# Kernel tuning notes

Measured on AMD Instinct MI355X. Metric: run time of the kernel, lower is better.

The kernel has to match this reference:

```python
import jax, jax.numpy as jnp
import numpy as np

EMBED = 1024
HEAD = 128

def setup_inputs() -> dict:
    key = jax.random.key(0)
    k1, k2, k3, k4 = jax.random.split(key, 4)
    x = jax.random.normal(k1, (4, 4096, EMBED), dtype=jnp.float32)
    # nn.Linear default init ~ U(-1/sqrt(fan_in), 1/sqrt(fan_in)); weights stored as [in, out] for x @ W
    s = 1.0 / np.sqrt(EMBED)
    Wq = jax.random.uniform(k2, (EMBED, HEAD), dtype=jnp.float32, minval=-s, maxval=s)
    Wk = jax.random.uniform(k3, (EMBED, HEAD), dtype=jnp.float32, minval=-s, maxval=s)
    Wv = jax.random.uniform(k4, (EMBED, HEAD), dtype=jnp.float32, minval=-s, maxval=s)
    return {"x": x, "Wq": Wq, "Wk": Wk, "Wv": Wv}

def reference(x, Wq, Wk, Wv):
    # x: [B, S, E]
    B, S, E = x.shape
    q = x @ Wq  # [B, S, H]
    k = x @ Wk
    v = x @ Wv
    scale = jnp.asarray(k.shape[-1], x.dtype) ** -0.5
    scores = jnp.einsum('bqh,bkh->bqk', q, k) * scale  # [B, S, S]
    causal = jnp.tril(jnp.ones((S, S), dtype=bool))
    scores = jnp.where(causal, scores, jnp.asarray(-jnp.inf, x.dtype))
    attn = jax.nn.softmax(scores, axis=-1)
    return jnp.einsum('bqk,bkh->bqh', attn, v)  # [B, S, H]
```

## Files before the change

kernel.cpp:

```cpp
#include <hip/hip_runtime.h>
#include <math.h>

#define BATCH 4
#define SEQ   4096
#define EMB   1024
#define HD    128
#define MROWS (BATCH*SEQ)
#define SCALE  0.08838834764831844f
#define SCALEQ 0.12751742f
#define CHUNK 10
#define NJOBS 119
#define MAXC  7

typedef __attribute__((ext_vector_type(8))) short bf16x8;
typedef __attribute__((ext_vector_type(4))) short short4v;
typedef __attribute__((ext_vector_type(4))) float f32x4;
typedef __attribute__((ext_vector_type(4))) int   i32x4;
typedef __attribute__((ext_vector_type(2))) int   i32x2;

static __device__ __forceinline__ unsigned short f2bf(float f) {
    unsigned int u = __float_as_uint(f);
    u += 0x7fff + ((u >> 16) & 1);
    return (unsigned short)(u >> 16);
}
static __device__ __forceinline__ float bf2f(unsigned short s) {
    return __uint_as_float((unsigned int)s << 16);
}
static __device__ __forceinline__ short4v pack4(float4 a) {
    short4v p;
    p[0] = (short)f2bf(a.x); p[1] = (short)f2bf(a.y);
    p[2] = (short)f2bf(a.z); p[3] = (short)f2bf(a.w);
    return p;
}
static __device__ __forceinline__ int cvtpk(float lo, float hi) {
    int r;
    asm("v_cvt_pk_bf16_f32 %0, %1, %2" : "=v"(r) : "v"(lo), "v"(hi));
    return r;
}
static __device__ __forceinline__ void gload_lds16(const unsigned short* g, unsigned short* l) {
    __builtin_amdgcn_global_load_lds(
        (const __attribute__((address_space(1))) void*)g,
        (__attribute__((address_space(3))) void*)l, 16, 0, 0);
}

__global__ __launch_bounds__(256) void wtrans_kernel(
    const float* __restrict__ Wq, const float* __restrict__ Wk,
    const float* __restrict__ Wv, unsigned short* __restrict__ Wt)
{
    __shared__ __align__(16) unsigned short Xs[16 * 132];
    const int w  = blockIdx.y;
    const float* W = (w == 0) ? Wq : (w == 1) ? Wk : Wv;
    const float sc = (w == 0) ? SCALEQ : 1.0f;
    const int bx = blockIdx.x;
    const int k0 = bx * 16;
    const int t  = threadIdx.x;

#pragma unroll
    for (int i = 0; i < 2; ++i) {
        int gg = i * 256 + t;
        int row = gg >> 5, c4 = gg & 31;
        float4 a = *(const float4*)&W[(size_t)(k0 + row) * HD + c4 * 4];
        short4v p;
        p[0] = (short)f2bf(a.x * sc); p[1] = (short)f2bf(a.y * sc);
        p[2] = (short)f2bf(a.z * sc); p[3] = (short)f2bf(a.w * sc);
        *(short4v*)&Xs[row * 132 + c4 * 4] = p;
    }
    __syncthreads();
    const int n = t >> 1, g = t & 1;
    i32x4 o;
#pragma unroll
    for (int e = 0; e < 4; ++e) {
        unsigned int lo = Xs[(g * 8 + e * 2    ) * 132 + n];
        unsigned int hi = Xs[(g * 8 + e * 2 + 1) * 132 + n];
        o[e] = (int)(lo | (hi << 16));
    }
    const int ntg  = w * 8 + (n >> 4);
    const int kc   = bx >> 1;
    const int quad = (bx * 2 + g) & 3;
    const int lane = quad * 16 + (n & 15);
    *(i32x4*)&Wt[(((size_t)ntg * 32 + kc) * 64 + lane) * 8] = o;
}

__global__ __launch_bounds__(512, 2) void qkv_kernel(
    const float* __restrict__ x, const unsigned short* __restrict__ Wt,
    unsigned short* __restrict__ qb, unsigned short* __restrict__ kb,
    unsigned short* __restrict__ vtb)
{
    __shared__ __align__(1024) unsigned short lds[58368];
    unsigned short* Ws  = lds;
    unsigned short* xsA = lds + 49152;
    unsigned short* xsB = lds + 53760;

    const int t    = threadIdx.x;
    const int lane = t & 63, ng = t >> 6;
    const int quad = lane >> 4, l16 = lane & 15;
    const int m0   = blockIdx.x * 64;

    f32x4 acc[4][3];
#pragma unroll
    for (int i = 0; i < 4; ++i)
#pragma unroll
        for (int j = 0; j < 3; ++j) acc[i][j] = (f32x4){0.f, 0.f, 0.f, 0.f};

    const int xr0 = t >> 4,         xc0 = (t & 15) * 4;
    const int xr1 = (t + 512) >> 4, xc1 = ((t + 512) & 15) * 4;
    const float* xb0 = x + (size_t)(m0 + xr0) * EMB + xc0;
    const float* xb1 = x + (size_t)(m0 + xr1) * EMB + xc1;

    const unsigned short* Wg = Wt + (size_t)lane * 8;
    float4 xra, xrb;

    {
        float4 a = *(const float4*)&xb0[0];
        float4 b = *(const float4*)&xb1[0];
        *(short4v*)&xsA[xr0 * 72 + xc0] = pack4(a);
        *(short4v*)&xsA[xr1 * 72 + xc1] = pack4(b);
#pragma unroll
        for (int jt = 0; jt < 3; ++jt)
#pragma unroll
            for (int kcl = 0; kcl < 2; ++kcl) {
                int ntg = ng * 3 + jt;
                gload_lds16(Wg + ((size_t)ntg * 32 + kcl) * 512,
                            Ws + ((size_t)ntg * 2 + kcl) * 512);
            }
        xra = *(const float4*)&xb0[64];
        xrb = *(const float4*)&xb1[64];
    }
    asm volatile("s_waitcnt vmcnt(2)" ::: "memory");
    asm volatile("s_waitcnt lgkmcnt(0)" ::: "memory");
    __builtin_amdgcn_s_barrier();

    for (int ph = 0; ph < 16; ++ph) {
        const int cb = ph & 1, nb = cb ^ 1;
        unsigned short* xc = cb ? xsB : xsA;
        unsigned short* xn = cb ? xsA : xsB;
        const int kcn = (ph < 15 ? ph + 1 : 15) * 2;

#pragma unroll
        for (int jt = 0; jt < 3; ++jt)
#pragma unroll
            for (int kcl = 0; kcl < 2; ++kcl) {
                int ntg = ng * 3 + jt;
                gload_lds16(Wg + ((size_t)ntg * 32 + kcn + kcl) * 512,
                            Ws + ((size_t)(nb * 48) + ntg * 2 + kcl) * 512);
            }
        *(short4v*)&xn[xr0 * 72 + xc0] = pack4(xra);
        *(short4v*)&xn[xr1 * 72 + xc1] = pack4(xrb);
        {
            const int xcol = (ph + 2 < 16) ? (ph + 2) * 64 : 960;
            xra = *(const float4*)&xb0[xcol];
            xrb = *(const float4*)&xb1[xcol];
        }
        {
            bf16x8 aA[2][4], aB[2][3];
#pragma unroll
            for (int ks = 0; ks < 2; ++ks)
#pragma unroll
                for (int jt = 0; jt < 3; ++jt)
                    aB[ks][jt] = *(const bf16x8*)&Ws[((size_t)(cb * 48) + (ng * 3 + jt) * 2 + ks) * 512 + lane * 8];
#pragma unroll
            for (int ks = 0; ks < 2; ++ks)
#pragma unroll
                for (int mt = 0; mt < 4; ++mt)
                    aA[ks][mt] = *(const bf16x8*)&xc[(mt * 16 + l16) * 72 + ks * 32 + quad * 8];
            __builtin_amdgcn_s_setprio(1);
#pragma unroll
            for (int ks = 0; ks < 2; ++ks)
#pragma unroll
                for (int mt = 0; mt < 4; ++mt)
#pragma unroll
                    for (int jt = 0; jt < 3; ++jt)
                        acc[mt][jt] = __builtin_amdgcn_mfma_f32_16x16x32_bf16(
                            aA[ks][mt], aB[ks][jt], acc[mt][jt], 0, 0, 0);
            __builtin_amdgcn_s_setprio(0);
        }
        asm volatile("s_waitcnt vmcnt(2)" ::: "memory");
        asm volatile("s_waitcnt lgkmcnt(0)" ::: "memory");
        __builtin_amdgcn_s_barrier();
    }

    unsigned short* Cq = lds;
    unsigned short* Ck = lds + 64 * 136;
    unsigned short* Cv = lds + 2 * 64 * 136;
#pragma unroll
    for (int mt = 0; mt < 4; ++mt)
#pragma unroll
        for (int jt = 0; jt < 3; ++jt) {
            int nt = ng * 3 + jt;
            int wm = nt >> 3, nl = nt & 7;
            if (wm < 2) {
                unsigned short* C = (wm == 0) ? Cq : Ck;
#pragma unroll
                for (int rr = 0; rr < 4; ++rr)
                    C[(mt * 16 + quad * 4 + rr) * 136 + nl * 16 + l16] =
                        f2bf(acc[mt][jt][rr]);
            } else {
                i32x2 p;
                p[0] = cvtpk(acc[mt][jt][0], acc[mt][jt][1]);
                p[1] = cvtpk(acc[mt][jt][2], acc[mt][jt][3]);
                *(i32x2*)&Cv[(nl * 16 + l16) * 72 + mt * 16 + quad * 4] = p;
            }
        }
    __syncthreads();
    {
#pragma unroll
        for (int i = 0; i < 2; ++i) {
            int idx = i * 512 + t;
            int row = idx >> 4, seg = idx & 15;
            *(i32x4*)&qb[((size_t)(m0 + row)) * HD + seg * 8] = *(const i32x4*)&Cq[row * 136 + seg * 8];
            *(i32x4*)&kb[((size_t)(m0 + row)) * HD + seg * 8] = *(const i32x4*)&Ck[row * 136 + seg * 8];
        }
    }
    {
        const int b = m0 >> 12, s0 = m0 & 4095;
#pragma unroll
        for (int i = 0; i < 2; ++i) {
            int idx = i * 512 + t;
            int h = idx >> 3, seg = idx & 7;
            *(i32x4*)&vtb[(size_t)b * (HD * SEQ) + (size_t)h * SEQ + s0 + seg * 8] =
                *(const i32x4*)&Cv[h * 72 + seg * 8];
        }
    }
}

#define PADK 136
#define PADV 72
#define PADP 72
#define DEFER_THR 8.0f

__global__ __launch_bounds__(256, 2) void flash_kernel(
    const unsigned short* __restrict__ qb, const unsigned short* __restrict__ kb,
    const unsigned short* __restrict__ vtb, unsigned short* __restrict__ Opart,
    float* __restrict__ mbuf, float* __restrict__ lbuf)
{
    __shared__ __align__(16) unsigned short Ks[64 * PADK];
    __shared__ __align__(16) unsigned short Vt[128 * PADV];
    __shared__ __align__(16) unsigned short Pt[128 * PADP];

    const int bx   = blockIdx.x;
    const int slot = bx & 7, pp = bx >> 3;
    const int b    = slot >> 1;
    const int jj   = pp * 2 + (slot & 1);
    if (jj >= NJOBS) return;

    const int t    = threadIdx.x;
    const int lane = t & 63, w = t >> 6;
    const int quad = lane >> 4, l16 = lane & 15;

    int qi = 0, s = 0;
    for (qi = 0; qi < 32; ++qi) {
        int cnt = (qi + 5) / 5;
        if (jj < s + cnt) break;
        s += cnt;
    }
    const int c     = jj - s;
    const int qrow0 = qi * 128 + w * 32 + l16;
    const int qrow1 = qrow0 + 16;
    const int jmax  = 2 * qi + 2;
    const int jbeg  = c * CHUNK;
    const int jend  = min(jbeg + CHUNK, jmax);
    const int wtop  = qi * 128 + w * 32;

    bf16x8 qf0[4], qf1[4];
    {
        const unsigned short* qp0 = qb + ((size_t)b * SEQ + qrow0) * HD;
        const unsigned short* qp1 = qb + ((size_t)b * SEQ + qrow1) * HD;
#pragma unroll
        for (int ks = 0; ks < 4; ++ks) {
            qf0[ks] = *(const bf16x8*)&qp0[ks * 32 + quad * 8];
            qf1[ks] = *(const bf16x8*)&qp1[ks * 32 + quad * 8];
        }
    }

    f32x4 O0[8], O1[8];
#pragma unroll
    for (int i = 0; i < 8; ++i) {
        O0[i] = (f32x4){0.f, 0.f, 0.f, 0.f};
        O1[i] = (f32x4){0.f, 0.f, 0.f, 0.f};
    }
    float m0r = -1e30f, l0r = 0.f, m1r = -1e30f, l1r = 0.f;

    const unsigned short* kbb  = kb  + (size_t)b * SEQ * HD;
    const unsigned short* vtbb = vtb + (size_t)b * HD * SEQ;

    i32x4 kr[4], vr[4];
#pragma unroll
    for (int i = 0; i < 4; ++i) {
        int gg = i * 256 + t;
        kr[i] = *(const i32x4*)&kbb[(size_t)jbeg * 64 * HD + (size_t)gg * 8];
        vr[i] = *(const i32x4*)&vtbb[(size_t)(gg >> 3) * SEQ + jbeg * 64 + (gg & 7) * 8];
    }

    for (int j0 = jbeg; j0 < jend; ++j0) {
        __syncthreads();
#pragma unroll
        for (int i = 0; i < 4; ++i) {
            int gg = i * 256 + t;
            *(i32x4*)&Ks[(gg >> 4) * PADK + (gg & 15) * 8] = kr[i];
            *(i32x4*)&Vt[(gg >> 3) * PADV + (gg & 7) * 8] = vr[i];
        }
        __syncthreads();

        if (j0 + 1 < jend) {
            const int j1 = j0 + 1;
#pragma unroll
            for (int i = 0; i < 4; ++i) {
                int gg = i * 256 + t;
                kr[i] = *(const i32x4*)&kbb[(size_t)j1 * 64 * HD + (size_t)gg * 8];
                vr[i] = *(const i32x4*)&vtbb[(size_t)(gg >> 3) * SEQ + j1 * 64 + (gg & 7) * 8];
            }
        }

        if (j0 * 64 > wtop + 31) continue;

        f32x4 st0[4], st1[4];
#pragma unroll
        for (int mt = 0; mt < 4; ++mt) {
            st0[mt] = (f32x4){0.f, 0.f, 0.f, 0.f};
            st1[mt] = (f32x4){0.f, 0.f, 0.f, 0.f};
        }
        __builtin_amdgcn_s_setprio(1);
#pragma unroll
        for (int mt = 0; mt < 4; ++mt)
#pragma unroll
            for (int ks = 0; ks < 4; ++ks) {
                bf16x8 kf = *(const bf16x8*)&Ks[(mt * 16 + l16) * PADK + ks * 32 + quad * 8];
                st0[mt] = __builtin_amdgcn_mfma_f32_16x16x32_bf16(kf, qf0[ks], st0[mt], 0, 0, 0);
                st1[mt] = __builtin_amdgcn_mfma_f32_16x16x32_bf16(kf, qf1[ks], st1[mt], 0, 0, 0);
            }
        __builtin_amdgcn_s_setprio(0);

        if (j0 * 64 + 63 > wtop) {
#pragma unroll
            for (int mt = 0; mt < 4; ++mt)
#pragma unroll
                for (int rr = 0; rr < 4; ++rr) {
                    int kv = j0 * 64 + mt * 16 + quad * 4 + rr;
                    if (kv > qrow0) st0[mt][rr] = -1e30f;
                    if (kv > qrow1) st1[mt][rr] = -1e30f;
                }
        }

        {
            float mx = -1e30f;
#pragma unroll
            for (int mt = 0; mt < 4; ++mt)
#pragma unroll
                for (int rr = 0; rr < 4; ++rr) mx = fmaxf(mx, st0[mt][rr]);
            mx = fmaxf(mx, __shfl_xor(mx, 16));
            mx = fmaxf(mx, __shfl_xor(mx, 32));
            if (!__all(mx <= m0r + DEFER_THR)) {
                const float m_new = fmaxf(m0r, mx);
                const float alpha = exp2f(m0r - m_new);
                l0r *= alpha;
#pragma unroll
                for (int i = 0; i < 8; ++i) {
                    O0[i][0] *= alpha; O0[i][1] *= alpha; O0[i][2] *= alpha; O0[i][3] *= alpha;
                }
                m0r = m_new;
            }
            float psum = 0.f;
#pragma unroll
            for (int mt = 0; mt < 4; ++mt)
#pragma unroll
                for (int rr = 0; rr < 4; ++rr) {
                    float p = exp2f(st0[mt][rr] - m0r);
                    st0[mt][rr] = p;
                    psum += p;
                }
            psum += __shfl_xor(psum, 16);
            psum += __shfl_xor(psum, 32);
            l0r += psum;
#pragma unroll
            for (int mt = 0; mt < 4; ++mt) {
                i32x2 p;
                p[0] = cvtpk(st0[mt][0], st0[mt][1]);
                p[1] = cvtpk(st0[mt][2], st0[mt][3]);
                *(i32x2*)&Pt[(w * 32 + l16) * PADP + mt * 16 + quad * 4] = p;
            }
        }
        {
            float mx = -1e30f;
#pragma unroll
            for (int mt = 0; mt < 4; ++mt)
#pragma unroll
                for (int rr = 0; rr < 4; ++rr) mx = fmaxf(mx, st1[mt][rr]);
            mx = fmaxf(mx, __shfl_xor(mx, 16));
            mx = fmaxf(mx, __shfl_xor(mx, 32));
            if (!__all(mx <= m1r + DEFER_THR)) {
                const float m_new = fmaxf(m1r, mx);
                const float alpha = exp2f(m1r - m_new);
                l1r *= alpha;
#pragma unroll
                for (int i = 0; i < 8; ++i) {
                    O1[i][0] *= alpha; O1[i][1] *= alpha; O1[i][2] *= alpha; O1[i][3] *= alpha;
                }
                m1r = m_new;
            }
            float psum = 0.f;
#pragma unroll
            for (int mt = 0; mt < 4; ++mt)
#pragma unroll
                for (int rr = 0; rr < 4; ++rr) {
                    float p = exp2f(st1[mt][rr] - m1r);
                    st1[mt][rr] = p;
                    psum += p;
                }
            psum += __shfl_xor(psum, 16);
            psum += __shfl_xor(psum, 32);
            l1r += psum;
#pragma unroll
            for (int mt = 0; mt < 4; ++mt) {
                i32x2 p;
                p[0] = cvtpk(st1[mt][0], st1[mt][1]);
                p[1] = cvtpk(st1[mt][2], st1[mt][3]);
                *(i32x2*)&Pt[(w * 32 + 16 + l16) * PADP + mt * 16 + quad * 4] = p;
            }
        }

        bf16x8 pf00 = *(const bf16x8*)&Pt[(w * 32 + l16) * PADP + quad * 8];
        bf16x8 pf01 = *(const bf16x8*)&Pt[(w * 32 + l16) * PADP + 32 + quad * 8];
        bf16x8 pf10 = *(const bf16x8*)&Pt[(w * 32 + 16 + l16) * PADP + quad * 8];
        bf16x8 pf11 = *(const bf16x8*)&Pt[(w * 32 + 16 + l16) * PADP + 32 + quad * 8];
        __builtin_amdgcn_s_setprio(1);
#pragma unroll
        for (int mt = 0; mt < 8; ++mt) {
            bf16x8 vf0 = *(const bf16x8*)&Vt[(mt * 16 + l16) * PADV + quad * 8];
            bf16x8 vf1 = *(const bf16x8*)&Vt[(mt * 16 + l16) * PADV + 32 + quad * 8];
            O0[mt] = __builtin_amdgcn_mfma_f32_16x16x32_bf16(vf0, pf00, O0[mt], 0, 0, 0);
            O0[mt] = __builtin_amdgcn_mfma_f32_16x16x32_bf16(vf1, pf01, O0[mt], 0, 0, 0);
            O1[mt] = __builtin_amdgcn_mfma_f32_16x16x32_bf16(vf0, pf10, O1[mt], 0, 0, 0);
            O1[mt] = __builtin_amdgcn_mfma_f32_16x16x32_bf16(vf1, pf11, O1[mt], 0, 0, 0);
        }
        __builtin_amdgcn_s_setprio(0);
    }

    const size_t jobbase = (size_t)b * NJOBS + jj;
    {
        const int r = w * 32 + l16;
        unsigned short* po = Opart + jobbase * (128 * 128) + (size_t)r * 128;
#pragma unroll
        for (int mt = 0; mt < 8; ++mt) {
            i32x2 p;
            p[0] = cvtpk(O0[mt][0], O0[mt][1]);
            p[1] = cvtpk(O0[mt][2], O0[mt][3]);
            *(i32x2*)&po[mt * 16 + quad * 4] = p;
        }
        if (quad == 0) {
            mbuf[jobbase * 128 + r] = m0r;
            lbuf[jobbase * 128 + r] = l0r;
        }
    }
    {
        const int r = w * 32 + 16 + l16;
        unsigned short* po = Opart + jobbase * (128 * 128) + (size_t)r * 128;
#pragma unroll
        for (int mt = 0; mt < 8; ++mt) {
            i32x2 p;
            p[0] = cvtpk(O1[mt][0], O1[mt][1]);
            p[1] = cvtpk(O1[mt][2], O1[mt][3]);
            *(i32x2*)&po[mt * 16 + quad * 4] = p;
        }
        if (quad == 0) {
            mbuf[jobbase * 128 + r] = m1r;
            lbuf[jobbase * 128 + r] = l1r;
        }
    }
}

__global__ __launch_bounds__(512) void combine_kernel(
    const unsigned short* __restrict__ Opart, const float* __restrict__ mbuf,
    const float* __restrict__ lbuf, float* __restrict__ out)
{
    const int qi = blockIdx.x, b = blockIdx.y;
    const int nc = (qi + 5) / 5;
    int j0 = 0;
    for (int q = 0; q < qi; ++q) j0 += (q + 5) / 5;
    const int t = threadIdx.x;
    const int row = blockIdx.z * 64 + (t >> 3);
    const int cg  = (t & 7) * 16;

    float mv[MAXC], lv[MAXC];
    float M = -1e30f;
#pragma unroll
    for (int c2 = 0; c2 < MAXC; ++c2) {
        if (c2 < nc) {
            const size_t jb = (size_t)b * NJOBS + j0 + c2;
            mv[c2] = mbuf[jb * 128 + row];
            lv[c2] = lbuf[jb * 128 + row];
            M = fmaxf(M, mv[c2]);
        } else { mv[c2] = -1e30f; lv[c2] = 0.f; }
    }
    float L = 0.f;
#pragma unroll
    for (int c2 = 0; c2 < MAXC; ++c2)
        if (c2 < nc) L += exp2f(mv[c2] - M) * lv[c2];
    const float Linv = 1.0f / L;

    float acc[16];
#pragma unroll
    for (int i = 0; i < 16; ++i) acc[i] = 0.f;
#pragma unroll
    for (int c2 = 0; c2 < MAXC; ++c2) {
        if (c2 < nc) {
            const float wgt = exp2f(mv[c2] - M) * Linv;
            const unsigned short* po = Opart + ((size_t)b * NJOBS + j0 + c2) * (128 * 128) +
                                       (size_t)row * 128 + cg;
#pragma unroll
            for (int i = 0; i < 2; ++i) {
                i32x4 d = *(const i32x4*)&po[i * 8];
#pragma unroll
                for (int e = 0; e < 4; ++e) {
                    unsigned int u = (unsigned int)d[e];
                    acc[i * 8 + e * 2]     = fmaf(wgt, bf2f((unsigned short)(u & 0xffff)), acc[i * 8 + e * 2]);
                    acc[i * 8 + e * 2 + 1] = fmaf(wgt, bf2f((unsigned short)(u >> 16)),   acc[i * 8 + e * 2 + 1]);
                }
            }
        }
    }
    float* op = out + ((size_t)b * SEQ + qi * 128 + row) * HD + cg;
#pragma unroll
    for (int i = 0; i < 4; ++i) {
        float4 res;
        res.x = acc[i * 4]; res.y = acc[i * 4 + 1];
        res.z = acc[i * 4 + 2]; res.w = acc[i * 4 + 3];
        *(float4*)&op[i * 4] = res;
    }
}

extern "C" void kernel_launch(void* const* d_in, const int* in_sizes, int n_in,
                              void* d_out, int out_size, void* d_ws, size_t ws_size,
                              hipStream_t stream) {
    const float* x  = (const float*)d_in[0];
    const float* Wq = (const float*)d_in[1];
    const float* Wk = (const float*)d_in[2];
    const float* Wv = (const float*)d_in[3];

    unsigned short* qb    = (unsigned short*)d_ws;
    unsigned short* kb    = qb  + (size_t)MROWS * HD;
    unsigned short* vtb   = kb  + (size_t)MROWS * HD;
    unsigned short* Wt    = vtb + (size_t)MROWS * HD;
    unsigned short* Opart = Wt  + (size_t)3 * HD * EMB;
    float* mbuf = (float*)(Opart + (size_t)BATCH * NJOBS * 128 * 128);
    float* lbuf = mbuf + (size_t)BATCH * NJOBS * 128;
    float* out = (float*)d_out;

    wtrans_kernel <<<dim3(64, 3),    dim3(256), 0, stream>>>(Wq, Wk, Wv, Wt);
    qkv_kernel    <<<dim3(256),      dim3(512), 0, stream>>>(x, Wt, qb, kb, vtb);
    flash_kernel  <<<dim3(480),      dim3(256), 0, stream>>>(qb, kb, vtb, Opart, mbuf, lbuf);
    combine_kernel<<<dim3(32, 4, 2), dim3(512), 0, stream>>>(Opart, mbuf, lbuf, out);
}
```

Before: 164.9 us.

## Halve QKV row tile to 32 and double grids for qkv and combine kernels

The QKV projection kernel now processes 32 rows per block instead of 64, which halves LDS and accumulators and doubles the grid to 512 blocks. Its k-loop is restructured into two half-steps, each with a single-slice W double buffer and its own barrier. The combine kernel likewise handles 32 rows per block with 8 columns per thread and launches twice as many blocks. The goal is better CU occupancy on a 256-CU part, at the cost of more W traffic per output row and more barriers.

```diff
diff --git a/kernel.cpp b/kernel.cpp
--- a/kernel.cpp
+++ b/kernel.cpp
@@ -86,104 +86,104 @@
     unsigned short* __restrict__ qb, unsigned short* __restrict__ kb,
     unsigned short* __restrict__ vtb)
 {
-    __shared__ __align__(1024) unsigned short lds[58368];
+    __shared__ __align__(1024) unsigned short lds[29184];
     unsigned short* Ws  = lds;
-    unsigned short* xsA = lds + 49152;
-    unsigned short* xsB = lds + 53760;
+    unsigned short* xsA = lds + 24576;
+    unsigned short* xsB = lds + 26880;
 
     const int t    = threadIdx.x;
     const int lane = t & 63, ng = t >> 6;
     const int quad = lane >> 4, l16 = lane & 15;
-    const int m0   = blockIdx.x * 64;
-
-    f32x4 acc[4][3];
-#pragma unroll
-    for (int i = 0; i < 4; ++i)
+    const int m0   = blockIdx.x * 32;
+    const int nt0  = ng * 3;
+
+    f32x4 acc[2][3];
+#pragma unroll
+    for (int i = 0; i < 2; ++i)
 #pragma unroll
         for (int j = 0; j < 3; ++j) acc[i][j] = (f32x4){0.f, 0.f, 0.f, 0.f};
 
-    const int xr0 = t >> 4,         xc0 = (t & 15) * 4;
-    const int xr1 = (t + 512) >> 4, xc1 = ((t + 512) & 15) * 4;
-    const float* xb0 = x + (size_t)(m0 + xr0) * EMB + xc0;
-    const float* xb1 = x + (size_t)(m0 + xr1) * EMB + xc1;
-
+    const int xrow = t >> 4, xseg = (t & 15) * 4;
+    const float* xbase = x + (size_t)(m0 + xrow) * EMB + xseg;
     const unsigned short* Wg = Wt + (size_t)lane * 8;
-    float4 xra, xrb;
-
+
+    float4 xr;
     {
-        float4 a = *(const float4*)&xb0[0];
-        float4 b = *(const float4*)&xb1[0];
-        *(short4v*)&xsA[xr0 * 72 + xc0] = pack4(a);
-        *(short4v*)&xsA[xr1 * 72 + xc1] = pack4(b);
+        float4 a = *(const float4*)&xbase[0];
+        *(short4v*)&xsA[xrow * 72 + xseg] = pack4(a);
 #pragma unroll
         for (int jt = 0; jt < 3; ++jt)
-#pragma unroll
-            for (int kcl = 0; kcl < 2; ++kcl) {
-                int ntg = ng * 3 + jt;
-                gload_lds16(Wg + ((size_t)ntg * 32 + kcl) * 512,
-                            Ws + ((size_t)ntg * 2 + kcl) * 512);
-            }
-        xra = *(const float4*)&xb0[64];
-        xrb = *(const float4*)&xb1[64];
-    }
-    asm volatile("s_waitcnt vmcnt(2)" ::: "memory");
+            gload_lds16(Wg + (size_t)((nt0 + jt) * 32) * 512,
+                        Ws + (size_t)(nt0 + jt) * 512);
+    }
+    asm volatile("s_waitcnt vmcnt(0)" ::: "memory");
     asm volatile("s_waitcnt lgkmcnt(0)" ::: "memory");
     __builtin_amdgcn_s_barrier();
 
-    for (int ph = 0; ph < 16; ++ph) {
-        const int cb = ph & 1, nb = cb ^ 1;
-        unsigned short* xc = cb ? xsB : xsA;
-        unsigned short* xn = cb ? xsA : xsB;
-        const int kcn = (ph < 15 ? ph + 1 : 15) * 2;
-
-#pragma unroll
-        for (int jt = 0; jt < 3; ++jt)
-#pragma unroll
-            for (int kcl = 0; kcl < 2; ++kcl) {
-                int ntg = ng * 3 + jt;
-                gload_lds16(Wg + ((size_t)ntg * 32 + kcn + kcl) * 512,
-                            Ws + ((size_t)(nb * 48) + ntg * 2 + kcl) * 512);
-            }
-        *(short4v*)&xn[xr0 * 72 + xc0] = pack4(xra);
-        *(short4v*)&xn[xr1 * 72 + xc1] = pack4(xrb);
+    for (int it = 0; it < 16; ++it) {
+        unsigned short* xc = (it & 1) ? xsB : xsA;
+        unsigned short* xn = (it & 1) ? xsA : xsB;
         {
-            const int xcol = (ph + 2 < 16) ? (ph + 2) * 64 : 960;
-            xra = *(const float4*)&xb0[xcol];
-            xrb = *(const float4*)&xb1[xcol];
+            const int kcn = 2 * it + 1;
+#pragma unroll
+            for (int jt = 0; jt < 3; ++jt)
+                gload_lds16(Wg + ((size_t)((nt0 + jt) * 32) + kcn) * 512,
+                            Ws + ((size_t)24 + nt0 + jt) * 512);
+            const int pc = (it + 1 < 16) ? it + 1 : 15;
+            xr = *(const float4*)&xbase[pc * 64];
+            bf16x8 aA[2], aB[3];
+#pragma unroll
+            for (int jt = 0; jt < 3; ++jt)
+                aB[jt] = *(const bf16x8*)&Ws[(size_t)(nt0 + jt) * 512 + lane * 8];
+#pragma unroll
+            for (int mt = 0; mt < 2; ++mt)
+                aA[mt] = *(const bf16x8*)&xc[(mt * 16 + l16) * 72 + quad * 8];
+            __builtin_amdgcn_s_setprio(1);
+#pragma unroll
+            for (int mt = 0; mt < 2; ++mt)
+#pragma unroll
+                for (int jt = 0; jt < 3; ++jt)
+                    acc[mt][jt] = __builtin_amdgcn_mfma_f32_16x16x32_bf16(
+                        aA[mt], aB[jt], acc[mt][jt], 0, 0, 0);
+            __builtin_amdgcn_s_setprio(0);
+            asm volatile("s_waitcnt vmcnt(1)" ::: "memory");
+            asm volatile("s_waitcnt lgkmcnt(0)" ::: "memory");
+            __builtin_amdgcn_s_barrier();
         }
         {
-            bf16x8 aA[2][4], aB[2][3];
-#pragma unroll
-            for (int ks = 0; ks < 2; ++ks)
+            const int kcn = (2 * it + 2 < 32) ? 2 * it + 2 : 31;
+#pragma unroll
+            for (int jt = 0; jt < 3; ++jt)
+                gload_lds16(Wg + ((size_t)((nt0 + jt) * 32) + kcn) * 512,
+                            Ws + (size_t)(nt0 + jt) * 512);
+            *(short4v*)&xn[xrow * 72 + xseg] = pack4(xr);
+            bf16x8 aA[2], aB[3];
+#pragma unroll
+            for (int jt = 0; jt < 3; ++jt)
+                aB[jt] = *(const bf16x8*)&Ws[((size_t)24 + nt0 + jt) * 512 + lane * 8];
+#pragma unroll
+            for (int mt = 0; mt < 2; ++mt)
+                aA[mt] = *(const bf16x8*)&xc[(mt * 16 + l16) * 72 + 32 + quad * 8];
+            __builtin_amdgcn_s_setprio(1);
+#pragma unroll
+            for (int mt = 0; mt < 2; ++mt)
 #pragma unroll
                 for (int jt = 0; jt < 3; ++jt)
-                    aB[ks][jt] = *(const bf16x8*)&Ws[((size_t)(cb * 48) + (ng * 3 + jt) * 2 + ks) * 512 + lane * 8];
-#pragma unroll
-            for (int ks = 0; ks < 2; ++ks)
-#pragma unroll
-                for (int mt = 0; mt < 4; ++mt)
-                    aA[ks][mt] = *(const bf16x8*)&xc[(mt * 16 + l16) * 72 + ks * 32 + quad * 8];
-            __builtin_amdgcn_s_setprio(1);
-#pragma unroll
-            for (int ks = 0; ks < 2; ++ks)
-#pragma unroll
-                for (int mt = 0; mt < 4; ++mt)
-#pragma unroll
-                    for (int jt = 0; jt < 3; ++jt)
-                        acc[mt][jt] = __builtin_amdgcn_mfma_f32_16x16x32_bf16(
-                            aA[ks][mt], aB[ks][jt], acc[mt][jt], 0, 0, 0);
+                    acc[mt][jt] = __builtin_amdgcn_mfma_f32_16x16x32_bf16(
+                        aA[mt], aB[jt], acc[mt][jt], 0, 0, 0);
             __builtin_amdgcn_s_setprio(0);
-        }
-        asm volatile("s_waitcnt vmcnt(2)" ::: "memory");
-        asm volatile("s_waitcnt lgkmcnt(0)" ::: "memory");
-        __builtin_amdgcn_s_barrier();
-    }
-
+            asm volatile("s_waitcnt vmcnt(0)" ::: "memory");
+            asm volatile("s_waitcnt lgkmcnt(0)" ::: "memory");
+            __builtin_amdgcn_s_barrier();
+        }
+    }
+
+    __syncthreads();
     unsigned short* Cq = lds;
-    unsigned short* Ck = lds + 64 * 136;
-    unsigned short* Cv = lds + 2 * 64 * 136;
-#pragma unroll
-    for (int mt = 0; mt < 4; ++mt)
+    unsigned short* Ck = lds + 32 * 136;
+    unsigned short* Cv = lds + 2 * 32 * 136;
+#pragma unroll
+    for (int mt = 0; mt < 2; ++mt)
 #pragma unroll
         for (int jt = 0; jt < 3; ++jt) {
             int nt = ng * 3 + jt;
@@ -198,28 +198,20 @@
                 i32x2 p;
                 p[0] = cvtpk(acc[mt][jt][0], acc[mt][jt][1]);
                 p[1] = cvtpk(acc[mt][jt][2], acc[mt][jt][3]);
-                *(i32x2*)&Cv[(nl * 16 + l16) * 72 + mt * 16 + quad * 4] = p;
+                *(i32x2*)&Cv[(nl * 16 + l16) * 40 + mt * 16 + quad * 4] = p;
             }
         }
     __syncthreads();
     {
-#pragma unroll
-        for (int i = 0; i < 2; ++i) {
-            int idx = i * 512 + t;
-            int row = idx >> 4, seg = idx & 15;
-            *(i32x4*)&qb[((size_t)(m0 + row)) * HD + seg * 8] = *(const i32x4*)&Cq[row * 136 + seg * 8];
-            *(i32x4*)&kb[((size_t)(m0 + row)) * HD + seg * 8] = *(const i32x4*)&Ck[row * 136 + seg * 8];
-        }
+        int row = t >> 4, seg = t & 15;
+        *(i32x4*)&qb[((size_t)(m0 + row)) * HD + seg * 8] = *(const i32x4*)&Cq[row * 136 + seg * 8];
+        *(i32x4*)&kb[((size_t)(m0 + row)) * HD + seg * 8] = *(const i32x4*)&Ck[row * 136 + seg * 8];
     }
     {
         const int b = m0 >> 12, s0 = m0 & 4095;
-#pragma unroll
-        for (int i = 0; i < 2; ++i) {
-            int idx = i * 512 + t;
-            int h = idx >> 3, seg = idx & 7;
-            *(i32x4*)&vtb[(size_t)b * (HD * SEQ) + (size_t)h * SEQ + s0 + seg * 8] =
-                *(const i32x4*)&Cv[h * 72 + seg * 8];
-        }
+        int h = t >> 2, seg = t & 3;
+        *(i32x4*)&vtb[(size_t)b * (HD * SEQ) + (size_t)h * SEQ + s0 + seg * 8] =
+            *(const i32x4*)&Cv[h * 40 + seg * 8];
     }
 }
 
@@ -477,8 +469,8 @@
     int j0 = 0;
     for (int q = 0; q < qi; ++q) j0 += (q + 5) / 5;
     const int t = threadIdx.x;
-    const int row = blockIdx.z * 64 + (t >> 3);
-    const int cg  = (t & 7) * 16;
+    const int row = blockIdx.z * 32 + (t >> 4);
+    const int cg  = (t & 15) * 8;
 
     float mv[MAXC], lv[MAXC];
     float M = -1e30f;
@@ -497,30 +489,27 @@
         if (c2 < nc) L += exp2f(mv[c2] - M) * lv[c2];
     const float Linv = 1.0f / L;
 
-    float acc[16];
-#pragma unroll
-    for (int i = 0; i < 16; ++i) acc[i] = 0.f;
+    float acc[8];
+#pragma unroll
+    for (int i = 0; i < 8; ++i) acc[i] = 0.f;
 #pragma unroll
     for (int c2 = 0; c2 < MAXC; ++c2) {
         if (c2 < nc) {
             const float wgt = exp2f(mv[c2] - M) * Linv;
             const unsigned short* po = Opart + ((size_t)b * NJOBS + j0 + c2) * (128 * 128) +
                                        (size_t)row * 128 + cg;
-#pragma unroll
-            for (int i = 0; i < 2; ++i) {
-                i32x4 d = *(const i32x4*)&po[i * 8];
-#pragma unroll
-                for (int e = 0; e < 4; ++e) {
-                    unsigned int u = (unsigned int)d[e];
-                    acc[i * 8 + e * 2]     = fmaf(wgt, bf2f((unsigned short)(u & 0xffff)), acc[i * 8 + e * 2]);
-                    acc[i * 8 + e * 2 + 1] = fmaf(wgt, bf2f((unsigned short)(u >> 16)),   acc[i * 8 + e * 2 + 1]);
-                }
+            i32x4 d = *(const i32x4*)&po[0];
+#pragma unroll
+            for (int e = 0; e < 4; ++e) {
+                unsigned int u = (unsigned int)d[e];
+                acc[e * 2]     = fmaf(wgt, bf2f((unsigned short)(u & 0xffff)), acc[e * 2]);
+                acc[e * 2 + 1] = fmaf(wgt, bf2f((unsigned short)(u >> 16)),   acc[e * 2 + 1]);
             }
         }
     }
     float* op = out + ((size_t)b * SEQ + qi * 128 + row) * HD + cg;
 #pragma unroll
-    for (int i = 0; i < 4; ++i) {
+    for (int i = 0; i < 2; ++i) {
         float4 res;
         res.x = acc[i * 4]; res.y = acc[i * 4 + 1];
         res.z = acc[i * 4 + 2]; res.w = acc[i * 4 + 3];
@@ -546,7 +535,7 @@
     float* out = (float*)d_out;
 
     wtrans_kernel <<<dim3(64, 3),    dim3(256), 0, stream>>>(Wq, Wk, Wv, Wt);
-    qkv_kernel    <<<dim3(256),      dim3(512), 0, stream>>>(x, Wt, qb, kb, vtb);
+    qkv_kernel    <<<dim3(512),      dim3(512), 0, stream>>>(x, Wt, qb, kb, vtb);
     flash_kernel  <<<dim3(480),      dim3(256), 0, stream>>>(qb, kb, vtb, Opart, mbuf, lbuf);
-    combine_kernel<<<dim3(32, 4, 2), dim3(512), 0, stream>>>(Opart, mbuf, lbuf, out);
-}
+    combine_kernel<<<dim3(32, 4, 4), dim3(512), 0, stream>>>(Opart, mbuf, lbuf, out);
+}
```

Result: no change. 166.9 us (+1.2%).
